# Optimization experiments

Hardware: AMD Instinct MI355X
Metric: run time of the kernel (lower is better)

Reference implementation:

```python
import jax, jax.numpy as jnp
import numpy as np

N_NODES = 50000
D = 128
E_RAND = 640000
ALPHA = 0.2  # LeakyReLU negative slope


def setup_inputs() -> dict:
    key = jax.random.key(0)
    k1, k2, k3, k4, k5 = jax.random.split(key, 5)
    inputs = jax.random.normal(k1, (N_NODES, D), dtype=jnp.float32) * 0.1
    # xavier_normal with gain=1.414 as in the torch module
    W = jax.random.normal(k2, (D, D), dtype=jnp.float32) * (1.414 * np.sqrt(2.0 / (D + D)))
    a = jax.random.normal(k3, (2 * D,), dtype=jnp.float32) * (1.414 * np.sqrt(2.0 / (1 + 2 * D)))
    # random edges + self-loops so every node has at least one outgoing edge (nonzero rowsum)
    src = jnp.concatenate([jax.random.randint(k4, (E_RAND,), 0, N_NODES), jnp.arange(N_NODES)])
    dst = jnp.concatenate([jax.random.randint(k5, (E_RAND,), 0, N_NODES), jnp.arange(N_NODES)])
    edge = jnp.stack([src, dst]).astype(jnp.int64)
    return {"inputs": inputs, "edge": edge, "W": W, "a": a}


def reference(inputs, edge, W, a):
    N = inputs.shape[0]
    src, dst = edge[0], edge[1]
    h = inputs @ W  # [N, D]
    # a @ [h_src; h_dst] per edge == h_src @ a[:D] + h_dst @ a[D:]
    score = h[src] @ a[:D] + h[dst] @ a[D:]  # [E]
    edge_e = jnp.exp(jax.nn.leaky_relu(score, negative_slope=ALPHA))  # [E]
    # sparse.mm(coo(edge, edge_e), ones): rowsum over src (coalesce sums duplicates)
    e_rowsum = jax.ops.segment_sum(edge_e, src, num_segments=N)  # [N]
    # sparse.mm(coo(edge, edge_e), h): weighted aggregation of h[dst] into src rows
    h_prime = jax.ops.segment_sum(edge_e[:, None] * h[dst], src, num_segments=N)  # [N, D]
    h_prime = h_prime / e_rowsum[:, None]
    return jax.nn.elu(h_prime)
```

## Files before the change

kernel.cpp:

```cpp
#include <hip/hip_runtime.h>
#include <hip/hip_bf16.h>


constexpr int D    = 128;
constexpr int CH   = 8192;
constexpr int CAPB = 1280;

typedef __attribute__((ext_vector_type(8))) short bf16x8;
typedef __attribute__((ext_vector_type(4))) float f32x4;

__device__ __forceinline__ float bf2f(short b) {
    return __uint_as_float(((unsigned)(unsigned short)b) << 16);
}
__device__ __forceinline__ short2 pk_bf16(float x, float y) {
    __hip_bfloat162 bb = __float22bfloat162_rn(make_float2(x, y));
    short2 r;
    __builtin_memcpy(&r, &bb, 4);
    return r;
}

__global__ __launch_bounds__(256) void bin_and_gemm(
    const float* __restrict__ X, const float* __restrict__ W,
    const float* __restrict__ a,
    const int* __restrict__ src, const int* __restrict__ dst,
    int* __restrict__ bcnt, int* __restrict__ binned,
    short* __restrict__ h, float* __restrict__ s1, float* __restrict__ s2,
    int NB, int NC, int N, int E) {
    __shared__ int hist[784], hbase[784];
    __shared__ short lbw[16384];
    if (blockIdx.x < (unsigned)NC) {
        const int c = blockIdx.x, t = threadIdx.x;
        for (int u = t; u < NB; u += 256) hist[u] = 0;
        __syncthreads();
        const int lo = c * CH, hi = min(lo + CH, E);
        const int hi4 = lo + ((hi - lo) & ~3);
        for (int i = lo + t * 4; i < hi4; i += 1024) {
            const int4 s4 = *(const int4*)(src + i);
            atomicAdd(&hist[s4.x >> 6], 1);
            atomicAdd(&hist[s4.y >> 6], 1);
            atomicAdd(&hist[s4.z >> 6], 1);
            atomicAdd(&hist[s4.w >> 6], 1);
        }
        for (int i = hi4 + t; i < hi; i += 256)
            atomicAdd(&hist[src[i] >> 6], 1);
        __syncthreads();
        for (int u = t; u < NB; u += 256) {
            hbase[u] = atomicAdd(&bcnt[u], hist[u]);
            hist[u] = 0;
        }
        __syncthreads();
        for (int i = lo + t * 4; i < hi4; i += 1024) {
            const int4 s4 = *(const int4*)(src + i);
            const int4 d4 = *(const int4*)(dst + i);
            const int sv[4] = {s4.x, s4.y, s4.z, s4.w};
            const int dv[4] = {d4.x, d4.y, d4.z, d4.w};
#pragma unroll
            for (int j = 0; j < 4; ++j) {
                const int b = sv[j] >> 6;
                const int r = atomicAdd(&hist[b], 1);
                const int idx = hbase[b] + r;
                if (idx < CAPB)
                    binned[b * CAPB + idx] = ((sv[j] & 63) << 16) | dv[j];
            }
        }
        for (int i = hi4 + t; i < hi; i += 256) {
            const int s = src[i];
            const int b = s >> 6;
            const int r = atomicAdd(&hist[b], 1);
            const int idx = hbase[b] + r;
            if (idx < CAPB)
                binned[b * CAPB + idx] = ((s & 63) << 16) | dst[i];
        }
        return;
    }
    for (int sl = threadIdx.x; sl < 2048; sl += 256) {
        const int l = sl & 63, st = sl >> 6;
        const int s = st >> 3, tt = st & 7;
        const int n = tt * 16 + (l & 15);
        const int q = l >> 4;
        const float* wp = W + (s * 32 + q * 8) * D + n;
        bf16x8 v;
#pragma unroll
        for (int jj = 0; jj < 4; ++jj) {
            const short2 p = pk_bf16(wp[(2 * jj) * D], wp[(2 * jj + 1) * D]);
            v[2 * jj]     = p.x;
            v[2 * jj + 1] = p.y;
        }
        *(bf16x8*)(lbw + sl * 8) = v;
    }
    __syncthreads();
    const int wave = threadIdx.x >> 6, lane = threadIdx.x & 63;
    const int r0 = (blockIdx.x - NC) * 64 + wave * 16;
    const int m = lane & 15, q = lane >> 4;
    const int arow = r0 + m;
    const bool rowok = arow < N;
    const float* xp = X + (size_t)arow * D + q * 8;

    f32x4 acc[8] = {};
#pragma unroll
    for (int s = 0; s < 4; ++s) {
        float4 xa = {0, 0, 0, 0}, xb = {0, 0, 0, 0};
        if (rowok) {
            xa = *(const float4*)(xp + s * 32);
            xb = *(const float4*)(xp + s * 32 + 4);
        }
        bf16x8 af;
        short2 c0 = pk_bf16(xa.x, xa.y), c1 = pk_bf16(xa.z, xa.w);
        short2 c2 = pk_bf16(xb.x, xb.y), c3 = pk_bf16(xb.z, xb.w);
        af[0] = c0.x; af[1] = c0.y; af[2] = c1.x; af[3] = c1.y;
        af[4] = c2.x; af[5] = c2.y; af[6] = c3.x; af[7] = c3.y;
#pragma unroll
        for (int t = 0; t < 8; ++t) {
            bf16x8 bf = *(const bf16x8*)(lbw + ((s * 8 + t) * 64 + lane) * 8);
            acc[t] = __builtin_amdgcn_mfma_f32_16x16x32_bf16(af, bf, acc[t], 0, 0, 0);
        }
    }
    float a1v[8], a2v[8];
#pragma unroll
    for (int t = 0; t < 8; ++t) {
        a1v[t] = a[t * 16 + m];
        a2v[t] = a[D + t * 16 + m];
    }
    float p1[4] = {0, 0, 0, 0}, p2[4] = {0, 0, 0, 0};
#pragma unroll
    for (int t = 0; t < 8; ++t) {
        short2 h01 = pk_bf16(acc[t][0], acc[t][1]);
        short2 h23 = pk_bf16(acc[t][2], acc[t][3]);
        const short hb[4] = {h01.x, h01.y, h23.x, h23.y};
#pragma unroll
        for (int i = 0; i < 4; ++i) {
            const int row = r0 + q * 4 + i;
            if (row < N) h[(size_t)row * D + t * 16 + m] = hb[i];
            const float hr = bf2f(hb[i]);
            p1[i] += hr * a1v[t];
            p2[i] += hr * a2v[t];
        }
    }
#pragma unroll
    for (int off = 1; off < 16; off <<= 1) {
#pragma unroll
        for (int i = 0; i < 4; ++i) {
            p1[i] += __shfl_xor(p1[i], off);
            p2[i] += __shfl_xor(p2[i], off);
        }
    }
    if (m < 4) {
        const int row = r0 + q * 4 + m;
        if (row < N) {
            const float v1 = (m == 0) ? p1[0] : (m == 1) ? p1[1] : (m == 2) ? p1[2] : p1[3];
            const float v2 = (m == 0) ? p2[0] : (m == 1) ? p2[1] : (m == 2) ? p2[2] : p2[3];
            s1[row] = v1;
            s2[row] = v2;
        }
    }
}

__global__ __launch_bounds__(512) void aggregate(
    const int* __restrict__ binned, const int* __restrict__ bcnt,
    const float* __restrict__ s1, const float* __restrict__ s2,
    const short* __restrict__ h, float* __restrict__ out, int N) {
    __shared__ int elist[CAPB];
    __shared__ unsigned short dlist[CAPB + 16];
    __shared__ int ncnt[64], exclp[64], pcnt[64];
    __shared__ float ss1[64];
    const int b = blockIdx.x, tid = threadIdx.x;
    const int n0 = b * 64;
    if (tid < 64) {
        ncnt[tid] = 0;
        pcnt[tid] = 0;
        ss1[tid] = (n0 + tid < N) ? s1[n0 + tid] : 0.f;
    }
    __syncthreads();
    const int nE = min(bcnt[b], CAPB);
    for (int i = tid; i < nE; i += 512) {
        const int e = binned[b * CAPB + i];
        elist[i] = e;
        atomicAdd(&ncnt[e >> 16], 1);
    }
    __syncthreads();
    if (tid < 64) {
        int v = ncnt[tid];
#pragma unroll
        for (int o = 1; o < 64; o <<= 1) {
            const int u = __shfl_up(v, o);
            if (tid >= o) v += u;
        }
        exclp[tid] = v - ncnt[tid];
    }
    __syncthreads();
    const int total = exclp[63] + ncnt[63];
    if (tid < 16) dlist[total + tid] = 0;
    for (int i = tid; i < nE; i += 512) {
        const int e = elist[i];
        const int r = e >> 16;
        const int k = atomicAdd(&pcnt[r], 1);
        dlist[exclp[r] + k] = (unsigned short)(e & 0xFFFF);
    }
    __syncthreads();

    const int wid = tid >> 6, lane = tid & 63;
    const int g = lane >> 4, m = lane & 15;
    const int m8 = m * 8;
#pragma unroll 1
    for (int t = 0; t < 8; ++t) {
        const int r = wid * 8 + t;
        const int n = n0 + r;
        if (n >= N) continue;
        const int cnt = ncnt[r];
        if (cnt == 0) continue;
        const int beg = exclp[r];
        const float s1n = ss1[r];

        int dA0 = dlist[beg + g];
        int dB0 = dlist[beg + 4 + g];
        float  sA0 = s2[dA0], sB0 = s2[dB0];
        bf16x8 rA0 = *(const bf16x8*)(h + (dA0 << 7) + m8);
        bf16x8 rB0 = *(const bf16x8*)(h + (dB0 << 7) + m8);

        float acc[8] = {};
        float rs = 0.f;
        for (int k0 = 0; k0 < cnt; k0 += 8) {
            const bool more = (k0 + 8) < cnt;
            float sA1, sB1;
            bf16x8 rA1, rB1;
            if (more) {
                const int dA1 = dlist[beg + k0 + 8 + g];
                const int dB1 = dlist[beg + k0 + 12 + g];
                sA1 = s2[dA1];
                sB1 = s2[dB1];
                rA1 = *(const bf16x8*)(h + (dA1 << 7) + m8);
                rB1 = *(const bf16x8*)(h + (dB1 << 7) + m8);
            }
            float scA = s1n + sA0;
            scA = scA > 0.f ? scA : 0.2f * scA;
            float eA = __expf(scA);
            if (k0 + g >= cnt) eA = 0.f;
            float scB = s1n + sB0;
            scB = scB > 0.f ? scB : 0.2f * scB;
            float eB = __expf(scB);
            if (k0 + 4 + g >= cnt) eB = 0.f;
#pragma unroll
            for (int j = 0; j < 8; ++j)
                acc[j] += eA * bf2f(rA0[j]) + eB * bf2f(rB0[j]);
            rs += eA + eB;
            if (more) { sA0 = sA1; sB0 = sB1; rA0 = rA1; rB0 = rB1; }
        }
#pragma unroll
        for (int off = 16; off <= 32; off <<= 1) {
            rs += __shfl_xor(rs, off);
#pragma unroll
            for (int j = 0; j < 8; ++j) acc[j] += __shfl_xor(acc[j], off);
        }
        if (g == 0) {
            const float inv = 1.f / rs;
            float o[8];
#pragma unroll
            for (int j = 0; j < 8; ++j) {
                const float v = acc[j] * inv;
                o[j] = v > 0.f ? v : __expf(v) - 1.f;
            }
            float* op = out + (size_t)n * D + m8;
            *(float4*)op       = make_float4(o[0], o[1], o[2], o[3]);
            *(float4*)(op + 4) = make_float4(o[4], o[5], o[6], o[7]);
        }
    }
}

extern "C" void kernel_launch(void* const* d_in, const int* in_sizes, int n_in,
                              void* d_out, int out_size, void* d_ws, size_t ws_size,
                              hipStream_t stream) {
    const float* X    = (const float*)d_in[0];
    const int*   edge = (const int*)d_in[1];
    const float* W    = (const float*)d_in[2];
    const float* a    = (const float*)d_in[3];
    float* out = (float*)d_out;

    const int N = in_sizes[0] / D;
    const int E = in_sizes[1] / 2;
    const int* src = edge;
    const int* dst = edge + E;

    const int NB = (N + 63) / 64;
    const int NC = (E + CH - 1) / CH;
    const int NG = (N + 63) / 64;

    char* ws = (char*)d_ws;
    short* h    = (short*)ws; ws += (size_t)N * D * sizeof(short);
    int* binned = (int*)ws;   ws += (size_t)NB * CAPB * sizeof(int);
    float* s1   = (float*)ws; ws += (size_t)N * sizeof(float);
    float* s2   = (float*)ws; ws += (size_t)N * sizeof(float);
    int* bcnt   = (int*)ws;   ws += (size_t)NB * sizeof(int);

    hipMemsetAsync(bcnt, 0, (size_t)NB * sizeof(int), stream);
    bin_and_gemm<<<NC + NG, 256, 0, stream>>>(X, W, a, src, dst, bcnt, binned,
                                              h, s1, s2, NB, NC, N, E);
    aggregate<<<NB, 512, 0, stream>>>(binned, bcnt, s1, s2, h, out, N);
}
```

Before: 135.2 us.

## Replace global-atomic binning with per-chunk LDS-sorted edges and descriptors

The binning blocks now sort their chunk of edges by destination bin in shared memory using a block-wide prefix scan. They write the sorted chunk contiguously to global memory, along with a per-chunk offset/count descriptor for each bin. This removes the global atomics on bin counters, the scattered global writes, and the memset launch. The aggregate kernel now scans 86 chunk descriptors and gathers many small segments per bin, which adds scan and gather overhead on that side. The W conversion is also rewritten to use coalesced float4 reads with a manual bf16 rounding.

```diff
diff --git a/kernel.cpp b/kernel.cpp
--- a/kernel.cpp
+++ b/kernel.cpp
@@ -9,6 +9,11 @@
 typedef __attribute__((ext_vector_type(8))) short bf16x8;
 typedef __attribute__((ext_vector_type(4))) float f32x4;
 
+__device__ __forceinline__ short f2bf(float f) {
+    unsigned u = __float_as_uint(f);
+    unsigned r = (u + 0x7fffu + ((u >> 16) & 1u)) >> 16;
+    return (short)r;
+}
 __device__ __forceinline__ float bf2f(short b) {
     return __uint_as_float(((unsigned)(unsigned short)b) << 16);
 }
@@ -23,17 +28,19 @@
     const float* __restrict__ X, const float* __restrict__ W,
     const float* __restrict__ a,
     const int* __restrict__ src, const int* __restrict__ dst,
-    int* __restrict__ bcnt, int* __restrict__ binned,
+    int* __restrict__ desc, int* __restrict__ binned,
     short* __restrict__ h, float* __restrict__ s1, float* __restrict__ s2,
     int NB, int NC, int N, int E) {
-    __shared__ int hist[784], hbase[784];
-    __shared__ short lbw[16384];
+    __shared__ int sbuf[CH];
+    __shared__ int hist[784];
+    __shared__ int sarr[1024];
     if (blockIdx.x < (unsigned)NC) {
         const int c = blockIdx.x, t = threadIdx.x;
         for (int u = t; u < NB; u += 256) hist[u] = 0;
         __syncthreads();
         const int lo = c * CH, hi = min(lo + CH, E);
-        const int hi4 = lo + ((hi - lo) & ~3);
+        const int len = hi - lo;
+        const int hi4 = lo + (len & ~3);
         for (int i = lo + t * 4; i < hi4; i += 1024) {
             const int4 s4 = *(const int4*)(src + i);
             atomicAdd(&hist[s4.x >> 6], 1);
@@ -44,8 +51,24 @@
         for (int i = hi4 + t; i < hi; i += 256)
             atomicAdd(&hist[src[i] >> 6], 1);
         __syncthreads();
+        for (int u = t; u < 1024; u += 256) sarr[u] = (u < NB) ? hist[u] : 0;
+        __syncthreads();
+        for (int o = 1; o < 1024; o <<= 1) {
+            int v[4];
+#pragma unroll
+            for (int k = 0; k < 4; ++k) {
+                const int idx = t + k * 256;
+                v[k] = (idx >= o) ? sarr[idx - o] : 0;
+            }
+            __syncthreads();
+#pragma unroll
+            for (int k = 0; k < 4; ++k) sarr[t + k * 256] += v[k];
+            __syncthreads();
+        }
         for (int u = t; u < NB; u += 256) {
-            hbase[u] = atomicAdd(&bcnt[u], hist[u]);
+            const int ex = sarr[u] - hist[u];
+            desc[(size_t)c * NB + u] = ex | (hist[u] << 14);
+            sarr[u] = ex;
             hist[u] = 0;
         }
         __syncthreads();
@@ -58,35 +81,36 @@
             for (int j = 0; j < 4; ++j) {
                 const int b = sv[j] >> 6;
                 const int r = atomicAdd(&hist[b], 1);
-                const int idx = hbase[b] + r;
-                if (idx < CAPB)
-                    binned[b * CAPB + idx] = ((sv[j] & 63) << 16) | dv[j];
+                sbuf[sarr[b] + r] = ((sv[j] & 63) << 16) | dv[j];
             }
         }
         for (int i = hi4 + t; i < hi; i += 256) {
             const int s = src[i];
             const int b = s >> 6;
             const int r = atomicAdd(&hist[b], 1);
-            const int idx = hbase[b] + r;
-            if (idx < CAPB)
-                binned[b * CAPB + idx] = ((s & 63) << 16) | dst[i];
-        }
+            sbuf[sarr[b] + r] = ((s & 63) << 16) | dst[i];
+        }
+        __syncthreads();
+        const int len4 = len & ~3;
+        for (int i = t * 4; i < len4; i += 1024)
+            *(int4*)(binned + (size_t)c * CH + i) = *(const int4*)(sbuf + i);
+        for (int i = len4 + t; i < len; i += 256)
+            binned[(size_t)c * CH + i] = sbuf[i];
         return;
     }
-    for (int sl = threadIdx.x; sl < 2048; sl += 256) {
-        const int l = sl & 63, st = sl >> 6;
-        const int s = st >> 3, tt = st & 7;
-        const int n = tt * 16 + (l & 15);
-        const int q = l >> 4;
-        const float* wp = W + (s * 32 + q * 8) * D + n;
-        bf16x8 v;
-#pragma unroll
-        for (int jj = 0; jj < 4; ++jj) {
-            const short2 p = pk_bf16(wp[(2 * jj) * D], wp[(2 * jj + 1) * D]);
-            v[2 * jj]     = p.x;
-            v[2 * jj + 1] = p.y;
-        }
-        *(bf16x8*)(lbw + sl * 8) = v;
+    short* lbw = (short*)sbuf;
+    for (int f4 = threadIdx.x; f4 < 4096; f4 += 256) {
+        const float4 w4 = *(const float4*)(W + f4 * 4);
+        const float wv[4] = {w4.x, w4.y, w4.z, w4.w};
+        const int f0 = f4 * 4;
+#pragma unroll
+        for (int u = 0; u < 4; ++u) {
+            const int f = f0 + u;
+            const int k = f >> 7, n = f & 127;
+            const int sl = ((k >> 5) * 8 + (n >> 4)) * 64 +
+                           ((k >> 3) & 3) * 16 + (n & 15);
+            lbw[sl * 8 + (k & 7)] = f2bf(wv[u]);
+        }
     }
     __syncthreads();
     const int wave = threadIdx.x >> 6, lane = threadIdx.x & 63;
@@ -156,11 +180,13 @@
 }
 
 __global__ __launch_bounds__(512) void aggregate(
-    const int* __restrict__ binned, const int* __restrict__ bcnt,
+    const int* __restrict__ binned, const int* __restrict__ desc,
     const float* __restrict__ s1, const float* __restrict__ s2,
-    const short* __restrict__ h, float* __restrict__ out, int N) {
+    const short* __restrict__ h, float* __restrict__ out,
+    int NB, int NC, int N) {
     __shared__ int elist[CAPB];
     __shared__ unsigned short dlist[CAPB + 16];
+    __shared__ int rdesc[128], sc[128];
     __shared__ int ncnt[64], exclp[64], pcnt[64];
     __shared__ float ss1[64];
     const int b = blockIdx.x, tid = threadIdx.x;
@@ -170,13 +196,36 @@
         pcnt[tid] = 0;
         ss1[tid] = (n0 + tid < N) ? s1[n0 + tid] : 0.f;
     }
-    __syncthreads();
-    const int nE = min(bcnt[b], CAPB);
-    for (int i = tid; i < nE; i += 512) {
-        const int e = binned[b * CAPB + i];
-        elist[i] = e;
-        atomicAdd(&ncnt[e >> 16], 1);
-    }
+    if (tid < 128) {
+        const int dsc = (tid < NC) ? desc[(size_t)tid * NB + b] : 0;
+        rdesc[tid] = dsc;
+        sc[tid] = (dsc >> 14) & 0x3FFF;
+    }
+    __syncthreads();
+    for (int o = 1; o < 128; o <<= 1) {
+        int v = 0;
+        if (tid < 128 && tid >= o) v = sc[tid - o];
+        __syncthreads();
+        if (tid < 128) sc[tid] += v;
+        __syncthreads();
+    }
+    const int total = sc[127];
+    const int nE = min(total, CAPB);
+    {
+        const int wid = tid >> 6, lane = tid & 63;
+        for (int c = wid; c < NC; c += 8) {
+            const int dsc = rdesc[c];
+            const int off = dsc & 0x3FFF;
+            const int cnt = (dsc >> 14) & 0x3FFF;
+            const int p0 = sc[c] - cnt;
+            for (int j = lane; j < cnt; j += 64) {
+                const int p = p0 + j;
+                if (p < CAPB) elist[p] = binned[(size_t)c * CH + off + j];
+            }
+        }
+    }
+    __syncthreads();
+    for (int i = tid; i < nE; i += 512) atomicAdd(&ncnt[elist[i] >> 16], 1);
     __syncthreads();
     if (tid < 64) {
         int v = ncnt[tid];
@@ -188,8 +237,8 @@
         exclp[tid] = v - ncnt[tid];
     }
     __syncthreads();
-    const int total = exclp[63] + ncnt[63];
-    if (tid < 16) dlist[total + tid] = 0;
+    const int tot2 = exclp[63] + ncnt[63];
+    if (tid < 16) dlist[tot2 + tid] = 0;
     for (int i = tid; i < nE; i += 512) {
         const int e = elist[i];
         const int r = e >> 16;
@@ -286,13 +335,12 @@
 
     char* ws = (char*)d_ws;
     short* h    = (short*)ws; ws += (size_t)N * D * sizeof(short);
-    int* binned = (int*)ws;   ws += (size_t)NB * CAPB * sizeof(int);
+    int* binned = (int*)ws;   ws += (size_t)NC * CH * sizeof(int);
+    int* desc   = (int*)ws;   ws += (size_t)NC * NB * sizeof(int);
     float* s1   = (float*)ws; ws += (size_t)N * sizeof(float);
     float* s2   = (float*)ws; ws += (size_t)N * sizeof(float);
-    int* bcnt   = (int*)ws;   ws += (size_t)NB * sizeof(int);
-
-    hipMemsetAsync(bcnt, 0, (size_t)NB * sizeof(int), stream);
-    bin_and_gemm<<<NC + NG, 256, 0, stream>>>(X, W, a, src, dst, bcnt, binned,
+
+    bin_and_gemm<<<NC + NG, 256, 0, stream>>>(X, W, a, src, dst, desc, binned,
                                               h, s1, s2, NB, NC, N, E);
-    aggregate<<<NB, 512, 0, stream>>>(binned, bcnt, s1, s2, h, out, N);
-}
+    aggregate<<<NB, 512, 0, stream>>>(binned, desc, s1, s2, h, out, NB, NC, N);
+}
```

Measured after the change: 141.0 us. 4.3% more time.
